# Optimization experiments

Hardware: AMD Instinct MI355X
Metric: run time of the kernel (lower is better)

## Reference

```python
import jax, jax.numpy as jnp
import numpy as np

BATCH, INPUTDIM, OUTDIM, GRIDSIZE = 4096, 256, 256, 64


def setup_inputs() -> dict:
    key = jax.random.key(0)
    k1, k2 = jax.random.split(key)
    x = jax.random.normal(k1, (BATCH, INPUTDIM), dtype=jnp.float32)
    # xavier_uniform over (2, outdim, inputdim, gridsize): fan_in = inputdim*gridsize, fan_out = outdim*gridsize
    fan_in = INPUTDIM * GRIDSIZE
    fan_out = OUTDIM * GRIDSIZE
    limit = float(np.sqrt(6.0 / (fan_in + fan_out)))
    fouriercoeffs = jax.random.uniform(
        k2, (2, OUTDIM, INPUTDIM, GRIDSIZE), dtype=jnp.float32,
        minval=-limit, maxval=limit)
    bias = jnp.zeros((1, OUTDIM), dtype=jnp.float32)
    return {"x": x, "fouriercoeffs": fouriercoeffs, "bias": bias}


def reference(x, fouriercoeffs, bias):
    # x: [B, inputdim]; fouriercoeffs: [2, outdim, inputdim, gridsize]; bias: [1, outdim]
    # gridsize_param is clamp/round'ed to an int in torch -> static = initial_gridsize here.
    G = fouriercoeffs.shape[-1]
    k = jnp.arange(1, G + 1, dtype=x.dtype)        # [G] frequencies 1..G
    xk = x[:, :, None] * k                          # [B, inputdim, G]
    c = jnp.cos(xk)                                 # [B, inputdim, G]
    s = jnp.sin(xk)                                 # [B, inputdim, G]
    # Fused contraction over (inputdim, gridsize) -- avoids the naive
    # [B, outdim, inputdim, gridsize] broadcast tensor of the torch code.
    y = (jnp.einsum('big,oig->bo', c, fouriercoeffs[0])
         + jnp.einsum('big,oig->bo', s, fouriercoeffs[1])
         + bias)                                    # [B, outdim]
    return y
```

## Files before the change

kernel.cpp:

```cpp
#include <hip/hip_runtime.h>
#include <hip/hip_bf16.h>


typedef __attribute__((ext_vector_type(8))) short short8;
typedef __attribute__((ext_vector_type(4))) float f32x4;

#define SPLITK 16
#define ICHUNK (256 / SPLITK)

#define INV2PI 0.15915494309189535f

__device__ __forceinline__ unsigned short f2bf(float f) {
    unsigned u = __builtin_bit_cast(unsigned, f);
    u += 0x7fffu + ((u >> 16) & 1u);
    return (unsigned short)(u >> 16);
}
#if __has_builtin(__builtin_amdgcn_cvt_pk_bf16_f32)
typedef __attribute__((ext_vector_type(2))) __bf16 bf16x2_t;
__device__ __forceinline__ unsigned pkbf16(float a, float b) {
    bf16x2_t v = __builtin_amdgcn_cvt_pk_bf16_f32(a, b);
    return __builtin_bit_cast(unsigned, v);
}
#else
__device__ __forceinline__ unsigned pkbf16(float a, float b) {
    unsigned ua = __builtin_bit_cast(unsigned, a) + 0x8000u;
    unsigned ub = __builtin_bit_cast(unsigned, b) + 0x8000u;
    return __builtin_amdgcn_perm(ub, ua, 0x07060302u);
}
#endif

__device__ __forceinline__ void dbl2(float c, float s, float& co, float& so) {
    float t = c + c;
    co = __builtin_fmaf(t, c, -1.f);
    so = t * s;
}
__device__ __forceinline__ void rot2(float c, float s, float cr, float sr,
                                     float& co, float& so) {
    float t = s * sr;
    co = __builtin_fmaf(c, cr, -t);
    float u = s * cr;
    so = __builtin_fmaf(c, sr, u);
}

__device__ __forceinline__ short8 chain8(float m1, float fm1, float f0) {
    unsigned r[4];
    float vp = fm1, v = f0;
    #pragma unroll
    for (int h = 0; h < 4; ++h) {
        float v1 = __builtin_fmaf(m1, v, -vp);
        r[h] = pkbf16(v, v1);
        float v2 = __builtin_fmaf(m1, v1, -v);
        vp = v1; v = v2;
    }
    uint4 u; u.x = r[0]; u.y = r[1]; u.z = r[2]; u.w = r[3];
    return __builtin_bit_cast(short8, u);
}

__device__ __forceinline__ void async_load16(const void* g, void* l) {
    __builtin_amdgcn_global_load_lds(
        (const __attribute__((address_space(1))) unsigned int*)g,
        (__attribute__((address_space(3))) unsigned int*)l,
        16, 0, 0);
}

__global__ __launch_bounds__(512) void prep_kernel(
    const float* __restrict__ fc, unsigned short* __restrict__ ws2)
{
    __shared__ unsigned pk[512][36];
    const int i = blockIdx.x;
    const int t = threadIdx.x;
    const int rr  = t >> 4;
    const int l16 = t & 15;

    #pragma unroll
    for (int p = 0; p < 16; ++p) {
        int r = p * 32 + rr;
        const float4* src =
            (const float4*)(fc + ((size_t)r * 256 + i) * 64) + l16;
        float4 v = *src;
        pk[r][l16 * 2]     = pkbf16(v.x, v.y);
        pk[r][l16 * 2 + 1] = pkbf16(v.z, v.w);
    }
    __syncthreads();

    #pragma unroll
    for (int gg = 0; gg < 8; ++gg) {
        int gi = gg * 512 + t;
        int sog = gi >> 6, ll = gi & 63;
        int s = sog >> 4, og = sog & 15;
        int o = og * 16 + (ll & 15);
        int k = s * 32 + (ll >> 4) * 8;
        int tt = k >> 6, g = k & 63;
        int r = tt * 256 + o;
        int c = g >> 1;
        uint4 v;
        v.x = pk[r][c]; v.y = pk[r][c + 1];
        v.z = pk[r][c + 2]; v.w = pk[r][c + 3];
        ((uint4*)ws2)[(size_t)i * 4096 + gi] = v;
    }
}

__global__ __launch_bounds__(256) void bias_init(
    const float* __restrict__ bias, float* __restrict__ out)
{
    int idx4 = blockIdx.x * 256 + threadIdx.x;
    ((float4*)out)[idx4] = ((const float4*)bias)[idx4 & 63];
}

__global__ __launch_bounds__(256) void reduce_kernel(
    const unsigned short* __restrict__ pws, const float* __restrict__ bias,
    float* __restrict__ out)
{
    int idx4 = blockIdx.x * 256 + threadIdx.x;
    float4 r = ((const float4*)bias)[idx4 & 63];
    #pragma unroll
    for (int z = 0; z < SPLITK; ++z) {
        ushort4 v = ((const ushort4*)pws)[(size_t)z * 262144 + idx4];
        r.x += __builtin_bit_cast(float, (unsigned)v.x << 16);
        r.y += __builtin_bit_cast(float, (unsigned)v.y << 16);
        r.z += __builtin_bit_cast(float, (unsigned)v.z << 16);
        r.w += __builtin_bit_cast(float, (unsigned)v.w << 16);
    }
    ((float4*)out)[idx4] = r;
}

template <bool USE_WS, bool PARTIAL>
__global__ __launch_bounds__(512, 2) void fkan_gemm(
    const float* __restrict__ x, const float* __restrict__ fc,
    const unsigned short* __restrict__ bws, float* __restrict__ out,
    unsigned short* __restrict__ pws)
{
    __shared__ uint4 Bimg[2][4096];
    __shared__ float xs[ICHUNK][256];

    const int t  = threadIdx.x;
    const int l  = t & 63;
    const int w  = t >> 6;
    const int q  = l >> 4;
    const int m  = l & 15;

    const int bid = blockIdx.x;
    const int z   = bid & 15;
    const int bx  = bid >> 4;
    const int rowBase = bx * 256;
    const int iBase   = z * ICHUNK;

    f32x4 acc[2][16];
    #pragma unroll
    for (int a = 0; a < 2; ++a)
        #pragma unroll
        for (int b = 0; b < 16; ++b) acc[a][b] = (f32x4)0.0f;

    auto stageB = [&](int p, int i) {
        if (USE_WS) {
            const uint4* base = (const uint4*)bws + (size_t)i * 4096;
            #pragma unroll
            for (int cc = 0; cc < 8; ++cc) {
                int c = cc * 8 + w;
                async_load16(base + (size_t)c * 64 + l, (void*)(&Bimg[p][c * 64]));
            }
        } else {
            #pragma unroll
            for (int gg = 0; gg < 8; ++gg) {
                int gi  = gg * 512 + t;
                int sog = gi >> 6, ll = gi & 63;
                int s = sog >> 4, ogb = sog & 15;
                int o = ogb * 16 + (ll & 15);
                int k = s * 32 + (ll >> 4) * 8;
                int tt = k >> 6, g = k & 63;
                const float4* p4 = (const float4*)(fc +
                    ((((size_t)tt * 256 + o) * 256 + i) * 64 + g));
                float4 a = p4[0], b = p4[1];
                uint4 v;
                v.x = pkbf16(a.x, a.y); v.y = pkbf16(a.z, a.w);
                v.z = pkbf16(b.x, b.y); v.w = pkbf16(b.z, b.w);
                Bimg[p][gi] = v;
            }
        }
    };

    stageB(0, iBase);
    {
        const int row = t >> 1;
        const int hf  = t & 1;
        const float4* px =
            (const float4*)(x + (size_t)(rowBase + row) * 256 + iBase) + hf * 2;
        float4 v0 = px[0], v1 = px[1];
        int c0 = hf * 8;
        xs[c0 + 0][row] = v0.x; xs[c0 + 1][row] = v0.y;
        xs[c0 + 2][row] = v0.z; xs[c0 + 3][row] = v0.w;
        xs[c0 + 4][row] = v1.x; xs[c0 + 5][row] = v1.y;
        xs[c0 + 6][row] = v1.z; xs[c0 + 7][row] = v1.w;
    }
    __syncthreads();

    #pragma unroll 1
    for (int ii = 0; ii < ICHUNK; ++ii) {
        const int p = ii & 1;

        if (ii + 1 < ICHUNK) stageB(p ^ 1, iBase + ii + 1);

        short8 aF[2][4];
        #pragma unroll
        for (int rf = 0; rf < 2; ++rf) {
            float xv = xs[ii][w * 32 + rf * 16 + m];
            float rev = xv * INV2PI;
            float s1 = __builtin_amdgcn_sinf(rev);
            float c1 = __builtin_amdgcn_cosf(rev);
            const float m1 = c1 + c1;
            float c2, s2, c4, s4, c8, s8, c16, s16, c32, s32;
            dbl2(c1, s1, c2, s2);
            dbl2(c2, s2, c4, s4);
            dbl2(c4, s4, c8, s8);
            dbl2(c8, s8, c16, s16);
            dbl2(c16, s16, c32, s32);
            float c24, s24;
            rot2(c16, s16, c8, s8, c24, s24);
            float cq = (q == 0) ? 1.f : (q == 1) ? c8 : (q == 2) ? c16 : c24;
            float sq = (q == 0) ? 0.f : (q == 1) ? s8 : (q == 2) ? s16 : s24;
            float cq1, sq1, cB, sB, cB1, sB1;
            rot2(cq, sq, c1, s1, cq1, sq1);
            rot2(cq, sq, c32, s32, cB, sB);
            rot2(cB, sB, c1, s1, cB1, sB1);
            aF[rf][0] = chain8(m1, cq, cq1);
            aF[rf][1] = chain8(m1, cB, cB1);
            aF[rf][2] = chain8(m1, sq, sq1);
            aF[rf][3] = chain8(m1, sB, sB1);
        }

        #pragma unroll
        for (int s = 0; s < 4; ++s) {
            #pragma unroll
            for (int hf = 0; hf < 2; ++hf) {
                short8 bF[8];
                #pragma unroll
                for (int cf = 0; cf < 8; ++cf)
                    bF[cf] = __builtin_bit_cast(short8,
                        Bimg[p][(s * 16 + hf * 8 + cf) * 64 + l]);
                #pragma unroll
                for (int rf = 0; rf < 2; ++rf)
                    #pragma unroll
                    for (int cf = 0; cf < 8; ++cf)
                        acc[rf][hf * 8 + cf] =
                            __builtin_amdgcn_mfma_f32_16x16x32_bf16(
                                aF[rf][s], bF[cf], acc[rf][hf * 8 + cf], 0, 0, 0);
            }
        }

        __syncthreads();
    }

    const int r0 = rowBase + w * 32 + (l >> 4) * 4;
    if (PARTIAL) {
        unsigned short* dst = pws + (size_t)z * (4096u * 256u);
        #pragma unroll
        for (int rf = 0; rf < 2; ++rf)
            #pragma unroll
            for (int cf = 0; cf < 16; ++cf)
                #pragma unroll
                for (int e = 0; e < 4; ++e)
                    dst[(size_t)(r0 + rf * 16 + e) * 256 + (cf * 16 + m)] =
                        f2bf(acc[rf][cf][e]);
    } else {
        #pragma unroll
        for (int rf = 0; rf < 2; ++rf)
            #pragma unroll
            for (int cf = 0; cf < 16; ++cf)
                #pragma unroll
                for (int e = 0; e < 4; ++e)
                    atomicAdd(out + (size_t)(r0 + rf * 16 + e) * 256 + (cf * 16 + m),
                              acc[rf][cf][e]);
    }
}

extern "C" void kernel_launch(void* const* d_in, const int* in_sizes, int n_in,
                              void* d_out, int out_size, void* d_ws, size_t ws_size,
                              hipStream_t stream) {
    const float* x    = (const float*)d_in[0];
    const float* fc   = (const float*)d_in[1];
    const float* bias = (const float*)d_in[2];
    float* out = (float*)d_out;
    unsigned short* bws = (unsigned short*)d_ws;

    const size_t wsCoeff = (size_t)256 * 4096 * 16;
    const size_t wsFull  = wsCoeff + (size_t)SPLITK * 4096 * 256 * 2;
    unsigned short* pws = (unsigned short*)((char*)d_ws + wsCoeff);

    if (ws_size >= wsFull) {
        hipLaunchKernelGGL(prep_kernel, dim3(256), dim3(512), 0, stream, fc, bws);
        hipLaunchKernelGGL((fkan_gemm<true, true>), dim3(256), dim3(512), 0, stream,
                           x, fc, bws, out, pws);
        hipLaunchKernelGGL(reduce_kernel, dim3(1024), dim3(256), 0, stream,
                           pws, bias, out);
    } else if (ws_size >= wsCoeff) {
        hipLaunchKernelGGL(bias_init, dim3(1024), dim3(256), 0, stream, bias, out);
        hipLaunchKernelGGL(prep_kernel, dim3(256), dim3(512), 0, stream, fc, bws);
        hipLaunchKernelGGL((fkan_gemm<true, false>), dim3(256), dim3(512), 0, stream,
                           x, fc, bws, out, pws);
    } else {
        hipLaunchKernelGGL(bias_init, dim3(1024), dim3(256), 0, stream, bias, out);
        hipLaunchKernelGGL((fkan_gemm<false, false>), dim3(256), dim3(512), 0, stream,
                           x, fc, bws, out, pws);
    }
}
```

Baseline: 148.9 us.

## Switch GEMM from 16x16x32 to 32x32x16 bf16 MFMA tiles

Replaces the 16x16x32 bf16 MFMA tiling with 32x32x16 MFMAs. Each wave now covers 32 rows by 256 columns with eight 16-float accumulators. The B-image layout in both the prep kernel and the inline staging path is rearranged to match the new operand format. The Fourier A-fragment generation is restructured so each lane computes one row's frequencies through repeated rotations by 16. The output store mapping changes to the 32x32 accumulator layout. The aim is fewer MFMA issues and fewer LDS B reads per FLOP, and fewer redundant sin/cos computations per lane. The risk is different register pressure and LDS access patterns.

```diff
diff --git a/kernel.cpp b/kernel.cpp
--- a/kernel.cpp
+++ b/kernel.cpp
@@ -3,7 +3,7 @@
 
 
 typedef __attribute__((ext_vector_type(8))) short short8;
-typedef __attribute__((ext_vector_type(4))) float f32x4;
+typedef __attribute__((ext_vector_type(16))) float f32x16;
 
 #define SPLITK 16
 #define ICHUNK (256 / SPLITK)
@@ -87,12 +87,12 @@
     for (int gg = 0; gg < 8; ++gg) {
         int gi = gg * 512 + t;
         int sog = gi >> 6, ll = gi & 63;
-        int s = sog >> 4, og = sog & 15;
-        int o = og * 16 + (ll & 15);
-        int k = s * 32 + (ll >> 4) * 8;
-        int tt = k >> 6, g = k & 63;
+        int ks = sog >> 3, cb = sog & 7;
+        int o  = cb * 32 + (ll & 31);
+        int kb = ks * 16 + (ll >> 5) * 8;
+        int tt = kb >> 6, g0 = kb & 63;
         int r = tt * 256 + o;
-        int c = g >> 1;
+        int c = g0 >> 1;
         uint4 v;
         v.x = pk[r][c]; v.y = pk[r][c + 1];
         v.z = pk[r][c + 2]; v.w = pk[r][c + 3];
@@ -136,8 +136,8 @@
     const int t  = threadIdx.x;
     const int l  = t & 63;
     const int w  = t >> 6;
-    const int q  = l >> 4;
-    const int m  = l & 15;
+    const int m32 = l & 31;
+    const int h  = l >> 5;
 
     const int bid = blockIdx.x;
     const int z   = bid & 15;
@@ -145,11 +145,9 @@
     const int rowBase = bx * 256;
     const int iBase   = z * ICHUNK;
 
-    f32x4 acc[2][16];
-    #pragma unroll
-    for (int a = 0; a < 2; ++a)
-        #pragma unroll
-        for (int b = 0; b < 16; ++b) acc[a][b] = (f32x4)0.0f;
+    f32x16 acc[8];
+    #pragma unroll
+    for (int a = 0; a < 8; ++a) acc[a] = (f32x16)0.0f;
 
     auto stageB = [&](int p, int i) {
         if (USE_WS) {
@@ -164,12 +162,12 @@
             for (int gg = 0; gg < 8; ++gg) {
                 int gi  = gg * 512 + t;
                 int sog = gi >> 6, ll = gi & 63;
-                int s = sog >> 4, ogb = sog & 15;
-                int o = ogb * 16 + (ll & 15);
-                int k = s * 32 + (ll >> 4) * 8;
-                int tt = k >> 6, g = k & 63;
+                int ks = sog >> 3, cb = sog & 7;
+                int o  = cb * 32 + (ll & 31);
+                int kb = ks * 16 + (ll >> 5) * 8;
+                int tt = kb >> 6, g0 = kb & 63;
                 const float4* p4 = (const float4*)(fc +
-                    ((((size_t)tt * 256 + o) * 256 + i) * 64 + g));
+                    ((((size_t)tt * 256 + o) * 256 + i) * 64 + g0));
                 float4 a = p4[0], b = p4[1];
                 uint4 v;
                 v.x = pkbf16(a.x, a.y); v.y = pkbf16(a.z, a.w);
@@ -200,76 +198,70 @@
 
         if (ii + 1 < ICHUNK) stageB(p ^ 1, iBase + ii + 1);
 
-        short8 aF[2][4];
-        #pragma unroll
-        for (int rf = 0; rf < 2; ++rf) {
-            float xv = xs[ii][w * 32 + rf * 16 + m];
+        short8 aF[8];
+        {
+            float xv = xs[ii][w * 32 + m32];
             float rev = xv * INV2PI;
             float s1 = __builtin_amdgcn_sinf(rev);
             float c1 = __builtin_amdgcn_cosf(rev);
             const float m1 = c1 + c1;
-            float c2, s2, c4, s4, c8, s8, c16, s16, c32, s32;
+            float c2, s2, c4, s4, c8, s8, c16, s16;
             dbl2(c1, s1, c2, s2);
             dbl2(c2, s2, c4, s4);
             dbl2(c4, s4, c8, s8);
             dbl2(c8, s8, c16, s16);
-            dbl2(c16, s16, c32, s32);
-            float c24, s24;
-            rot2(c16, s16, c8, s8, c24, s24);
-            float cq = (q == 0) ? 1.f : (q == 1) ? c8 : (q == 2) ? c16 : c24;
-            float sq = (q == 0) ? 0.f : (q == 1) ? s8 : (q == 2) ? s16 : s24;
-            float cq1, sq1, cB, sB, cB1, sB1;
-            rot2(cq, sq, c1, s1, cq1, sq1);
-            rot2(cq, sq, c32, s32, cB, sB);
-            rot2(cB, sB, c1, s1, cB1, sB1);
-            aF[rf][0] = chain8(m1, cq, cq1);
-            aF[rf][1] = chain8(m1, cB, cB1);
-            aF[rf][2] = chain8(m1, sq, sq1);
-            aF[rf][3] = chain8(m1, sB, sB1);
+            float cB = h ? c8 : 1.f;
+            float sB = h ? s8 : 0.f;
+            #pragma unroll
+            for (int k = 0; k < 4; ++k) {
+                float cB1, sB1;
+                rot2(cB, sB, c1, s1, cB1, sB1);
+                aF[k]     = chain8(m1, cB, cB1);
+                aF[4 + k] = chain8(m1, sB, sB1);
+                if (k < 3) {
+                    float cN, sN;
+                    rot2(cB, sB, c16, s16, cN, sN);
+                    cB = cN; sB = sN;
+                }
+            }
         }
 
         #pragma unroll
-        for (int s = 0; s < 4; ++s) {
-            #pragma unroll
-            for (int hf = 0; hf < 2; ++hf) {
-                short8 bF[8];
-                #pragma unroll
-                for (int cf = 0; cf < 8; ++cf)
-                    bF[cf] = __builtin_bit_cast(short8,
-                        Bimg[p][(s * 16 + hf * 8 + cf) * 64 + l]);
-                #pragma unroll
-                for (int rf = 0; rf < 2; ++rf)
-                    #pragma unroll
-                    for (int cf = 0; cf < 8; ++cf)
-                        acc[rf][hf * 8 + cf] =
-                            __builtin_amdgcn_mfma_f32_16x16x32_bf16(
-                                aF[rf][s], bF[cf], acc[rf][hf * 8 + cf], 0, 0, 0);
-            }
+        for (int ks = 0; ks < 8; ++ks) {
+            short8 bF[8];
+            #pragma unroll
+            for (int cf = 0; cf < 8; ++cf)
+                bF[cf] = __builtin_bit_cast(short8,
+                    Bimg[p][(ks * 8 + cf) * 64 + l]);
+            #pragma unroll
+            for (int cf = 0; cf < 8; ++cf)
+                acc[cf] = __builtin_amdgcn_mfma_f32_32x32x16_bf16(
+                    aF[ks], bF[cf], acc[cf], 0, 0, 0);
         }
 
         __syncthreads();
     }
 
-    const int r0 = rowBase + w * 32 + (l >> 4) * 4;
+    const int r0 = rowBase + w * 32 + h * 4;
     if (PARTIAL) {
         unsigned short* dst = pws + (size_t)z * (4096u * 256u);
         #pragma unroll
-        for (int rf = 0; rf < 2; ++rf)
-            #pragma unroll
-            for (int cf = 0; cf < 16; ++cf)
-                #pragma unroll
-                for (int e = 0; e < 4; ++e)
-                    dst[(size_t)(r0 + rf * 16 + e) * 256 + (cf * 16 + m)] =
-                        f2bf(acc[rf][cf][e]);
+        for (int cf = 0; cf < 8; ++cf)
+            #pragma unroll
+            for (int e = 0; e < 16; ++e) {
+                int rl = (e & 3) + 8 * (e >> 2);
+                dst[(size_t)(r0 + rl) * 256 + (cf * 32 + m32)] =
+                    f2bf(acc[cf][e]);
+            }
     } else {
         #pragma unroll
-        for (int rf = 0; rf < 2; ++rf)
-            #pragma unroll
-            for (int cf = 0; cf < 16; ++cf)
-                #pragma unroll
-                for (int e = 0; e < 4; ++e)
-                    atomicAdd(out + (size_t)(r0 + rf * 16 + e) * 256 + (cf * 16 + m),
-                              acc[rf][cf][e]);
+        for (int cf = 0; cf < 8; ++cf)
+            #pragma unroll
+            for (int e = 0; e < 16; ++e) {
+                int rl = (e & 3) + 8 * (e >> 2);
+                atomicAdd(out + (size_t)(r0 + rl) * 256 + (cf * 32 + m32),
+                          acc[cf][e]);
+            }
     }
 }
 
```

After: 150.8 us. Within noise of the previous version (+1.3%).

## Fuse prep, GEMM and reduce into one cooperative kernel with grid syncs

Applied to the files above, without the earlier changes.

Replaces the three-launch path (coefficient repack, split-K GEMM, partial reduction) with a single cooperative kernel that uses grid-wide syncs between the phases. Shared memory is unioned so the repack buffer and GEMM tiles reuse the same LDS. The aim is to remove two kernel launch gaps and the tail idle time between kernels. In exchange it adds two grid barriers and relies on all 256 blocks of 512 threads being co-resident, which the cooperative launch requires.

```diff
diff --git a/kernel.cpp b/kernel.cpp
--- a/kernel.cpp
+++ b/kernel.cpp
@@ -1,5 +1,8 @@
 #include <hip/hip_runtime.h>
 #include <hip/hip_bf16.h>
+#include <hip/hip_cooperative_groups.h>
+
+namespace cg = cooperative_groups;
 
 
 typedef __attribute__((ext_vector_type(8))) short short8;
@@ -62,6 +65,7 @@
         (__attribute__((address_space(3))) unsigned int*)l,
         16, 0, 0);
 }
+
 
 __global__ __launch_bounds__(512) void prep_kernel(
     const float* __restrict__ fc, unsigned short* __restrict__ ws2)
@@ -88,11 +92,11 @@
         int gi = gg * 512 + t;
         int sog = gi >> 6, ll = gi & 63;
         int s = sog >> 4, og = sog & 15;
-        int o = og * 16 + (ll & 15);
-        int k = s * 32 + (ll >> 4) * 8;
-        int tt = k >> 6, g = k & 63;
+        int o  = og * 16 + (ll & 15);
+        int k  = s * 32 + (ll >> 4) * 8;
+        int tt = k >> 6, g0 = k & 63;
         int r = tt * 256 + o;
-        int c = g >> 1;
+        int c = g0 >> 1;
         uint4 v;
         v.x = pk[r][c]; v.y = pk[r][c + 1];
         v.z = pk[r][c + 2]; v.w = pk[r][c + 3];
@@ -124,11 +128,190 @@
     ((float4*)out)[idx4] = r;
 }
 
-template <bool USE_WS, bool PARTIAL>
+union FusedSM {
+    struct { uint4 Bimg[2][4096]; float xs[ICHUNK][256]; } g;
+    unsigned pk[512][36];
+};
+
+__global__ __launch_bounds__(512, 2) void fkan_fused(
+    const float* __restrict__ x, const float* __restrict__ fc,
+    const float* __restrict__ bias, unsigned short* __restrict__ bws,
+    unsigned short* __restrict__ pws, float* __restrict__ out)
+{
+    __shared__ FusedSM sm;
+    const int t = threadIdx.x;
+
+    {
+        const int i = blockIdx.x;
+        const int rr  = t >> 4;
+        const int l16 = t & 15;
+        #pragma unroll
+        for (int p = 0; p < 16; ++p) {
+            int r = p * 32 + rr;
+            const float4* src =
+                (const float4*)(fc + ((size_t)r * 256 + i) * 64) + l16;
+            float4 v = *src;
+            sm.pk[r][l16 * 2]     = pkbf16(v.x, v.y);
+            sm.pk[r][l16 * 2 + 1] = pkbf16(v.z, v.w);
+        }
+        __syncthreads();
+        #pragma unroll
+        for (int gg = 0; gg < 8; ++gg) {
+            int gi = gg * 512 + t;
+            int sog = gi >> 6, ll = gi & 63;
+            int s = sog >> 4, og = sog & 15;
+            int o  = og * 16 + (ll & 15);
+            int k  = s * 32 + (ll >> 4) * 8;
+            int tt = k >> 6, g0 = k & 63;
+            int r = tt * 256 + o;
+            int c = g0 >> 1;
+            uint4 v;
+            v.x = sm.pk[r][c]; v.y = sm.pk[r][c + 1];
+            v.z = sm.pk[r][c + 2]; v.w = sm.pk[r][c + 3];
+            ((uint4*)bws)[(size_t)i * 4096 + gi] = v;
+        }
+    }
+    __threadfence();
+    cg::this_grid().sync();
+
+    {
+        uint4 (*Bimg)[4096] = sm.g.Bimg;
+        float (*xs)[256]    = sm.g.xs;
+
+        const int l  = t & 63;
+        const int w  = t >> 6;
+        const int q  = l >> 4;
+        const int m  = l & 15;
+
+        const int bid = blockIdx.x;
+        const int z   = bid & 15;
+        const int bx  = bid >> 4;
+        const int rowBase = bx * 256;
+        const int iBase   = z * ICHUNK;
+
+        f32x4 acc[2][16];
+        #pragma unroll
+        for (int a = 0; a < 2; ++a)
+            #pragma unroll
+            for (int b = 0; b < 16; ++b) acc[a][b] = (f32x4)0.0f;
+
+        auto stageB = [&](int p, int i) {
+            const uint4* base = (const uint4*)bws + (size_t)i * 4096;
+            #pragma unroll
+            for (int cc = 0; cc < 8; ++cc) {
+                int c = cc * 8 + w;
+                async_load16(base + (size_t)c * 64 + l, (void*)(&Bimg[p][c * 64]));
+            }
+        };
+
+        stageB(0, iBase);
+        {
+            const int row = t >> 1;
+            const int hf  = t & 1;
+            const float4* px =
+                (const float4*)(x + (size_t)(rowBase + row) * 256 + iBase) + hf * 2;
+            float4 v0 = px[0], v1 = px[1];
+            int c0 = hf * 8;
+            xs[c0 + 0][row] = v0.x; xs[c0 + 1][row] = v0.y;
+            xs[c0 + 2][row] = v0.z; xs[c0 + 3][row] = v0.w;
+            xs[c0 + 4][row] = v1.x; xs[c0 + 5][row] = v1.y;
+            xs[c0 + 6][row] = v1.z; xs[c0 + 7][row] = v1.w;
+        }
+        __syncthreads();
+
+        #pragma unroll 1
+        for (int ii = 0; ii < ICHUNK; ++ii) {
+            const int p = ii & 1;
+
+            if (ii + 1 < ICHUNK) stageB(p ^ 1, iBase + ii + 1);
+
+            short8 aF[2][4];
+            #pragma unroll
+            for (int rf = 0; rf < 2; ++rf) {
+                float xv = xs[ii][w * 32 + rf * 16 + m];
+                float rev = xv * INV2PI;
+                float s1 = __builtin_amdgcn_sinf(rev);
+                float c1 = __builtin_amdgcn_cosf(rev);
+                const float m1 = c1 + c1;
+                float c2, s2, c4, s4, c8, s8, c16, s16, c32, s32;
+                dbl2(c1, s1, c2, s2);
+                dbl2(c2, s2, c4, s4);
+                dbl2(c4, s4, c8, s8);
+                dbl2(c8, s8, c16, s16);
+                dbl2(c16, s16, c32, s32);
+                float c24, s24;
+                rot2(c16, s16, c8, s8, c24, s24);
+                float cq = (q == 0) ? 1.f : (q == 1) ? c8 : (q == 2) ? c16 : c24;
+                float sq = (q == 0) ? 0.f : (q == 1) ? s8 : (q == 2) ? s16 : s24;
+                float cq1, sq1, cB, sB, cB1, sB1;
+                rot2(cq, sq, c1, s1, cq1, sq1);
+                rot2(cq, sq, c32, s32, cB, sB);
+                rot2(cB, sB, c1, s1, cB1, sB1);
+                aF[rf][0] = chain8(m1, cq, cq1);
+                aF[rf][1] = chain8(m1, cB, cB1);
+                aF[rf][2] = chain8(m1, sq, sq1);
+                aF[rf][3] = chain8(m1, sB, sB1);
+            }
+
+            #pragma unroll
+            for (int s = 0; s < 4; ++s) {
+                #pragma unroll
+                for (int hf = 0; hf < 2; ++hf) {
+                    short8 bF[8];
+                    #pragma unroll
+                    for (int cf = 0; cf < 8; ++cf)
+                        bF[cf] = __builtin_bit_cast(short8,
+                            Bimg[p][(s * 16 + hf * 8 + cf) * 64 + l]);
+                    #pragma unroll
+                    for (int rf = 0; rf < 2; ++rf)
+                        #pragma unroll
+                        for (int cf = 0; cf < 8; ++cf)
+                            acc[rf][hf * 8 + cf] =
+                                __builtin_amdgcn_mfma_f32_16x16x32_bf16(
+                                    aF[rf][s], bF[cf], acc[rf][hf * 8 + cf],
+                                    0, 0, 0);
+                }
+            }
+
+            __syncthreads();
+        }
+
+        const int r0 = rowBase + w * 32 + (l >> 4) * 4;
+        unsigned short* dst = pws + (size_t)z * (4096u * 256u);
+        #pragma unroll
+        for (int rf = 0; rf < 2; ++rf)
+            #pragma unroll
+            for (int cf = 0; cf < 16; ++cf)
+                #pragma unroll
+                for (int e = 0; e < 4; ++e)
+                    dst[(size_t)(r0 + rf * 16 + e) * 256 + (cf * 16 + m)] =
+                        f2bf(acc[rf][cf][e]);
+    }
+    __threadfence();
+    cg::this_grid().sync();
+
+    {
+        #pragma unroll
+        for (int rep = 0; rep < 2; ++rep) {
+            int idx4 = rep * 131072 + blockIdx.x * 512 + t;
+            float4 r = ((const float4*)bias)[idx4 & 63];
+            #pragma unroll
+            for (int z = 0; z < SPLITK; ++z) {
+                ushort4 v = ((const ushort4*)pws)[(size_t)z * 262144 + idx4];
+                r.x += __builtin_bit_cast(float, (unsigned)v.x << 16);
+                r.y += __builtin_bit_cast(float, (unsigned)v.y << 16);
+                r.z += __builtin_bit_cast(float, (unsigned)v.z << 16);
+                r.w += __builtin_bit_cast(float, (unsigned)v.w << 16);
+            }
+            ((float4*)out)[idx4] = r;
+        }
+    }
+}
+
+template <bool USE_WS>
 __global__ __launch_bounds__(512, 2) void fkan_gemm(
     const float* __restrict__ x, const float* __restrict__ fc,
-    const unsigned short* __restrict__ bws, float* __restrict__ out,
-    unsigned short* __restrict__ pws)
+    const unsigned short* __restrict__ bws, float* __restrict__ out)
 {
     __shared__ uint4 Bimg[2][4096];
     __shared__ float xs[ICHUNK][256];
@@ -197,7 +380,6 @@
     #pragma unroll 1
     for (int ii = 0; ii < ICHUNK; ++ii) {
         const int p = ii & 1;
-
         if (ii + 1 < ICHUNK) stageB(p ^ 1, iBase + ii + 1);
 
         short8 aF[2][4];
@@ -246,31 +428,18 @@
                                 aF[rf][s], bF[cf], acc[rf][hf * 8 + cf], 0, 0, 0);
             }
         }
-
         __syncthreads();
     }
 
     const int r0 = rowBase + w * 32 + (l >> 4) * 4;
-    if (PARTIAL) {
-        unsigned short* dst = pws + (size_t)z * (4096u * 256u);
-        #pragma unroll
-        for (int rf = 0; rf < 2; ++rf)
-            #pragma unroll
-            for (int cf = 0; cf < 16; ++cf)
-                #pragma unroll
-                for (int e = 0; e < 4; ++e)
-                    dst[(size_t)(r0 + rf * 16 + e) * 256 + (cf * 16 + m)] =
-                        f2bf(acc[rf][cf][e]);
-    } else {
-        #pragma unroll
-        for (int rf = 0; rf < 2; ++rf)
-            #pragma unroll
-            for (int cf = 0; cf < 16; ++cf)
-                #pragma unroll
-                for (int e = 0; e < 4; ++e)
-                    atomicAdd(out + (size_t)(r0 + rf * 16 + e) * 256 + (cf * 16 + m),
-                              acc[rf][cf][e]);
-    }
+    #pragma unroll
+    for (int rf = 0; rf < 2; ++rf)
+        #pragma unroll
+        for (int cf = 0; cf < 16; ++cf)
+            #pragma unroll
+            for (int e = 0; e < 4; ++e)
+                atomicAdd(out + (size_t)(r0 + rf * 16 + e) * 256 + (cf * 16 + m),
+                          acc[rf][cf][e]);
 }
 
 extern "C" void kernel_launch(void* const* d_in, const int* in_sizes, int n_in,
@@ -287,19 +456,18 @@
     unsigned short* pws = (unsigned short*)((char*)d_ws + wsCoeff);
 
     if (ws_size >= wsFull) {
-        hipLaunchKernelGGL(prep_kernel, dim3(256), dim3(512), 0, stream, fc, bws);
-        hipLaunchKernelGGL((fkan_gemm<true, true>), dim3(256), dim3(512), 0, stream,
-                           x, fc, bws, out, pws);
-        hipLaunchKernelGGL(reduce_kernel, dim3(1024), dim3(256), 0, stream,
-                           pws, bias, out);
+        void* args[] = {(void*)&x, (void*)&fc, (void*)&bias,
+                        (void*)&bws, (void*)&pws, (void*)&out};
+        hipLaunchCooperativeKernel((const void*)fkan_fused,
+                                   dim3(256), dim3(512), args, 0, stream);
     } else if (ws_size >= wsCoeff) {
         hipLaunchKernelGGL(bias_init, dim3(1024), dim3(256), 0, stream, bias, out);
         hipLaunchKernelGGL(prep_kernel, dim3(256), dim3(512), 0, stream, fc, bws);
-        hipLaunchKernelGGL((fkan_gemm<true, false>), dim3(256), dim3(512), 0, stream,
-                           x, fc, bws, out, pws);
+        hipLaunchKernelGGL((fkan_gemm<true>), dim3(256), dim3(512), 0, stream,
+                           x, fc, bws, out);
     } else {
         hipLaunchKernelGGL(bias_init, dim3(1024), dim3(256), 0, stream, bias, out);
-        hipLaunchKernelGGL((fkan_gemm<false, false>), dim3(256), dim3(512), 0, stream,
-                           x, fc, bws, out, pws);
-    }
-}
+        hipLaunchKernelGGL((fkan_gemm<false>), dim3(256), dim3(512), 0, stream,
+                           x, fc, bws, out);
+    }
+}
```

Measured after the change: 333.1 us. +123.7%, slower.

## Split GEMM tile into 128x128 blocks with 256 threads and 1024-block grid

Applied to the files above, without the earlier changes.

Shrinks the per-block output tile from 256 rows by 256 columns to 128 rows by 128 columns. The block drops from 512 to 256 threads and the grid grows from 256 to 1024 blocks, with a new by index choosing the column half. This is meant to raise parallelism and occupancy on a GPU with many CUs, since the old 256-block grid left CUs underused, and it halves LDS and accumulator use per block. In exchange, the sin/cos A-fragment work and the x staging are repeated for both column halves, and each B chunk feeds fewer MFMAs.

```diff
diff --git a/kernel.cpp b/kernel.cpp
--- a/kernel.cpp
+++ b/kernel.cpp
@@ -88,11 +88,11 @@
         int gi = gg * 512 + t;
         int sog = gi >> 6, ll = gi & 63;
         int s = sog >> 4, og = sog & 15;
-        int o = og * 16 + (ll & 15);
-        int k = s * 32 + (ll >> 4) * 8;
-        int tt = k >> 6, g = k & 63;
+        int o  = og * 16 + (ll & 15);
+        int k  = s * 32 + (ll >> 4) * 8;
+        int tt = k >> 6, g0 = k & 63;
         int r = tt * 256 + o;
-        int c = g >> 1;
+        int c = g0 >> 1;
         uint4 v;
         v.x = pk[r][c]; v.y = pk[r][c + 1];
         v.z = pk[r][c + 2]; v.w = pk[r][c + 3];
@@ -125,13 +125,13 @@
 }
 
 template <bool USE_WS, bool PARTIAL>
-__global__ __launch_bounds__(512, 2) void fkan_gemm(
+__global__ __launch_bounds__(256, 2) void fkan_gemm(
     const float* __restrict__ x, const float* __restrict__ fc,
     const unsigned short* __restrict__ bws, float* __restrict__ out,
     unsigned short* __restrict__ pws)
 {
-    __shared__ uint4 Bimg[2][4096];
-    __shared__ float xs[ICHUNK][256];
+    __shared__ uint4 Bimg[2][2048];
+    __shared__ float xs[ICHUNK][128];
 
     const int t  = threadIdx.x;
     const int l  = t & 63;
@@ -141,31 +141,34 @@
 
     const int bid = blockIdx.x;
     const int z   = bid & 15;
-    const int bx  = bid >> 4;
-    const int rowBase = bx * 256;
+    const int by  = (bid >> 4) & 1;
+    const int bx  = bid >> 5;
+    const int rowBase = bx * 128;
     const int iBase   = z * ICHUNK;
 
-    f32x4 acc[2][16];
+    f32x4 acc[2][8];
     #pragma unroll
     for (int a = 0; a < 2; ++a)
         #pragma unroll
-        for (int b = 0; b < 16; ++b) acc[a][b] = (f32x4)0.0f;
+        for (int b = 0; b < 8; ++b) acc[a][b] = (f32x4)0.0f;
 
     auto stageB = [&](int p, int i) {
         if (USE_WS) {
             const uint4* base = (const uint4*)bws + (size_t)i * 4096;
             #pragma unroll
             for (int cc = 0; cc < 8; ++cc) {
-                int c = cc * 8 + w;
-                async_load16(base + (size_t)c * 64 + l, (void*)(&Bimg[p][c * 64]));
+                int cl = cc * 4 + w;
+                int sog = (cl >> 3) * 16 + by * 8 + (cl & 7);
+                async_load16(base + (size_t)sog * 64 + l,
+                             (void*)(&Bimg[p][cl * 64]));
             }
         } else {
             #pragma unroll
             for (int gg = 0; gg < 8; ++gg) {
-                int gi  = gg * 512 + t;
-                int sog = gi >> 6, ll = gi & 63;
-                int s = sog >> 4, ogb = sog & 15;
-                int o = ogb * 16 + (ll & 15);
+                int gi  = gg * 256 + t;
+                int sogl = gi >> 6, ll = gi & 63;
+                int s = sogl >> 3, ogl = sogl & 7;
+                int o = (by * 8 + ogl) * 16 + (ll & 15);
                 int k = s * 32 + (ll >> 4) * 8;
                 int tt = k >> 6, g = k & 63;
                 const float4* p4 = (const float4*)(fc +
@@ -230,45 +233,42 @@
 
         #pragma unroll
         for (int s = 0; s < 4; ++s) {
-            #pragma unroll
-            for (int hf = 0; hf < 2; ++hf) {
-                short8 bF[8];
+            short8 bF[8];
+            #pragma unroll
+            for (int cf = 0; cf < 8; ++cf)
+                bF[cf] = __builtin_bit_cast(short8,
+                    Bimg[p][(s * 8 + cf) * 64 + l]);
+            #pragma unroll
+            for (int rf = 0; rf < 2; ++rf)
                 #pragma unroll
                 for (int cf = 0; cf < 8; ++cf)
-                    bF[cf] = __builtin_bit_cast(short8,
-                        Bimg[p][(s * 16 + hf * 8 + cf) * 64 + l]);
-                #pragma unroll
-                for (int rf = 0; rf < 2; ++rf)
-                    #pragma unroll
-                    for (int cf = 0; cf < 8; ++cf)
-                        acc[rf][hf * 8 + cf] =
-                            __builtin_amdgcn_mfma_f32_16x16x32_bf16(
-                                aF[rf][s], bF[cf], acc[rf][hf * 8 + cf], 0, 0, 0);
-            }
+                    acc[rf][cf] = __builtin_amdgcn_mfma_f32_16x16x32_bf16(
+                        aF[rf][s], bF[cf], acc[rf][cf], 0, 0, 0);
         }
 
         __syncthreads();
     }
 
     const int r0 = rowBase + w * 32 + (l >> 4) * 4;
+    const int c0 = by * 128 + m;
     if (PARTIAL) {
         unsigned short* dst = pws + (size_t)z * (4096u * 256u);
         #pragma unroll
         for (int rf = 0; rf < 2; ++rf)
             #pragma unroll
-            for (int cf = 0; cf < 16; ++cf)
+            for (int cf = 0; cf < 8; ++cf)
                 #pragma unroll
                 for (int e = 0; e < 4; ++e)
-                    dst[(size_t)(r0 + rf * 16 + e) * 256 + (cf * 16 + m)] =
+                    dst[(size_t)(r0 + rf * 16 + e) * 256 + (c0 + cf * 16)] =
                         f2bf(acc[rf][cf][e]);
     } else {
         #pragma unroll
         for (int rf = 0; rf < 2; ++rf)
             #pragma unroll
-            for (int cf = 0; cf < 16; ++cf)
+            for (int cf = 0; cf < 8; ++cf)
                 #pragma unroll
                 for (int e = 0; e < 4; ++e)
-                    atomicAdd(out + (size_t)(r0 + rf * 16 + e) * 256 + (cf * 16 + m),
+                    atomicAdd(out + (size_t)(r0 + rf * 16 + e) * 256 + (c0 + cf * 16),
                               acc[rf][cf][e]);
     }
 }
@@ -288,18 +288,18 @@
 
     if (ws_size >= wsFull) {
         hipLaunchKernelGGL(prep_kernel, dim3(256), dim3(512), 0, stream, fc, bws);
-        hipLaunchKernelGGL((fkan_gemm<true, true>), dim3(256), dim3(512), 0, stream,
+        hipLaunchKernelGGL((fkan_gemm<true, true>), dim3(1024), dim3(256), 0, stream,
                            x, fc, bws, out, pws);
         hipLaunchKernelGGL(reduce_kernel, dim3(1024), dim3(256), 0, stream,
                            pws, bias, out);
     } else if (ws_size >= wsCoeff) {
         hipLaunchKernelGGL(bias_init, dim3(1024), dim3(256), 0, stream, bias, out);
         hipLaunchKernelGGL(prep_kernel, dim3(256), dim3(512), 0, stream, fc, bws);
-        hipLaunchKernelGGL((fkan_gemm<true, false>), dim3(256), dim3(512), 0, stream,
+        hipLaunchKernelGGL((fkan_gemm<true, false>), dim3(1024), dim3(256), 0, stream,
                            x, fc, bws, out, pws);
     } else {
         hipLaunchKernelGGL(bias_init, dim3(1024), dim3(256), 0, stream, bias, out);
-        hipLaunchKernelGGL((fkan_gemm<false, false>), dim3(256), dim3(512), 0, stream,
+        hipLaunchKernelGGL((fkan_gemm<false, false>), dim3(1024), dim3(256), 0, stream,
                            x, fc, bws, out, pws);
     }
 }
```

Result: slower. 156.5 us (+5.1%).
